# Optimization experiments

Measured on AMD Instinct MI355X. Metric: run time of the kernel, lower is better.

The kernel has to match this reference:

```python
import jax, jax.numpy as jnp
import numpy as np

E, A, K = 8192, 128, 512  # parallel_envs, num_agents, passengers per env
P = E * K                 # total passengers (global table rows)


def setup_inputs() -> dict:
    key = jax.random.key(0)
    k1, k2, k3, k4, k5, k6 = jax.random.split(key, 6)
    passengers = jax.random.normal(k1, (P, 11), dtype=jnp.float32)
    # column 0 is the env index of each passenger (used to gather timesteps)
    passengers = passengers.at[:, 0].set(jnp.repeat(jnp.arange(E, dtype=jnp.float32), K))
    accepts = jax.random.bernoulli(k2, 0.5, (E, A))
    picks = jax.random.bernoulli(k3, 0.3, (E, A))
    # env-partitioned global passenger indices: row e targets in [e*K, (e+1)*K)
    local_t = jax.random.randint(k4, (E, A), 0, K, dtype=jnp.int32)
    targets = jnp.arange(E, dtype=jnp.int32)[:, None] * K + local_t
    vectors = jax.random.normal(k5, (E, A, 4), dtype=jnp.float32)
    # give a quarter of agents zero src->dst distance so the pick branch fires
    vectors = vectors.at[:, : A // 4, 2:4].set(vectors[:, : A // 4, 0:2])
    # mark last 8 agent slots per env as invalid (all -100)
    vectors = vectors.at[:, -8:, :].set(-100.0)
    timesteps = jax.random.randint(k6, (E,), 0, 1000, dtype=jnp.int32)
    return {"passengers": passengers, "accepts": accepts, "picks": picks,
            "targets": targets, "vectors": vectors, "timesteps": timesteps}


def _distances(vectors):
    d = jnp.sqrt(((vectors[:, :, 0:2] - vectors[:, :, 2:4]) ** 2).sum(-1))
    return jnp.where((vectors == -100.0).all(-1), jnp.inf, d)


def _dup_mask(t, P):
    # torch: unique(return_inverse, return_counts) -> counts[inverse] > 1 & t != -100
    seg = jnp.where(t >= 0, t, P).ravel()  # -100 -> sentinel bucket P
    counts = jax.ops.segment_sum(jnp.ones(seg.shape, jnp.int32), seg, num_segments=P + 1)
    return (counts[seg].reshape(t.shape) > 1) & (t >= 0)


def reference(passengers, accepts, picks, targets, vectors, timesteps):
    E_, A_ = targets.shape
    P_ = passengers.shape[0]

    distances = _distances(vectors)
    accept_t = jnp.where(accepts, targets, -100)

    def cond(carry):
        t, _ = carry
        return _dup_mask(t, P_).any()

    def body(carry):
        t, d = carry
        dup = _dup_mask(t, P_)
        d = jnp.where(dup, d, jnp.inf)  # cumulative, as in torch
        keep = jnp.arange(A_)[None, :] == jnp.argmin(d, axis=1)[:, None]
        t = jnp.where(dup & ~keep, -100, t)
        return t, d

    accept_t, _ = jax.lax.while_loop(cond, body, (accept_t, distances))

    # scatter accept results into passenger table (at most one agent per passenger now)
    valid = accept_t >= 0
    seg = jnp.where(valid, accept_t, P_).ravel()
    accepted = jax.ops.segment_sum(valid.astype(jnp.int32).ravel(), seg, num_segments=P_ + 1)[:P_] > 0
    agent_ids = jnp.broadcast_to(jnp.arange(A_, dtype=jnp.int32)[None, :], (E_, A_))
    agent_of = jax.ops.segment_max(jnp.where(valid, agent_ids, -100).ravel(), seg, num_segments=P_ + 1)[:P_]
    ts = timesteps[passengers[:, 0].astype(jnp.int32)].astype(passengers.dtype)  # per-passenger timestep

    p = passengers
    p = p.at[:, 6].set(jnp.where(accepted, 1.0, p[:, 6]))
    p = p.at[:, 9].set(jnp.where(accepted, ts, p[:, 9]))
    p = p.at[:, 7].set(jnp.where(accepted, agent_of.astype(p.dtype), p[:, 7]))

    # pick transition: only zero-distance picks succeed
    d2 = _distances(vectors)
    pick_t = jnp.where(picks, targets, -100)
    pd = jnp.where(pick_t >= 0, d2, jnp.inf)
    pick_t = jnp.where(pd < 1e-6, pick_t, -100)
    pvalid = pick_t >= 0
    pseg = jnp.where(pvalid, pick_t, P_).ravel()
    picked = jax.ops.segment_sum(pvalid.astype(jnp.int32).ravel(), pseg, num_segments=P_ + 1)[:P_] > 0
    p = p.at[:, 6].set(jnp.where(picked, 2.0, p[:, 6]))
    p = p.at[:, 10].set(jnp.where(picked, ts, p[:, 10]))
    return p
```

## Files before the change

### kernel.cpp

```cpp
#include <hip/hip_runtime.h>

#define E_ENV 8192
#define A_AG  128
#define K_PASS 512
#define P_TOT (E_ENV * K_PASS)
#define N4    (P_TOT * 11 / 4)

__global__ __launch_bounds__(256) void k_copy(
    const float4* __restrict__ in, float4* __restrict__ out)
{
    int tid = blockIdx.x * 256 + threadIdx.x;
    out[tid] = in[tid];
}

__global__ __launch_bounds__(128) void k_env(
    const int* __restrict__ accepts, const int* __restrict__ picks,
    const int* __restrict__ targets, const float4* __restrict__ vectors,
    const int* __restrict__ timesteps, float* __restrict__ out)
{
    __shared__ int cnt[K_PASS];
    __shared__ float swv[2];
    __shared__ int   swi[2];

    const int e   = blockIdx.x;
    const int a   = threadIdx.x;
    const int gid = e * A_AG + a;

    #pragma unroll
    for (int j = 0; j < K_PASS / A_AG; ++j)
        cnt[a + j * A_AG] = 0;
    __syncthreads();

    float4 v = vectors[gid];
    bool invalid = (v.x == -100.0f) && (v.y == -100.0f) &&
                   (v.z == -100.0f) && (v.w == -100.0f);
    float dx = v.x - v.z, dy = v.y - v.w;
    float d = sqrtf(dx * dx + dy * dy);
    if (invalid) d = INFINITY;

    const int t     = targets[gid];
    const int tl    = t - e * K_PASS;
    const bool acc  = accepts[gid] != 0;
    const bool pick = picks[gid] != 0;

    int at = acc ? t : -100;
    if (at >= 0) atomicAdd(&cnt[tl], 1);
    __syncthreads();

    bool dup = (at >= 0) && (cnt[tl] > 1);
    float bv = dup ? d : INFINITY;
    int   bi = a;

    #pragma unroll
    for (int off = 32; off > 0; off >>= 1) {
        float ov = __shfl_xor(bv, off);
        int   oi = __shfl_xor(bi, off);
        if (ov < bv || (ov == bv && oi < bi)) { bv = ov; bi = oi; }
    }
    int wave = a >> 6;
    if ((a & 63) == 0) { swv[wave] = bv; swi[wave] = bi; }
    __syncthreads();
    float v0 = swv[0], v1 = swv[1];
    int   i0 = swi[0], i1 = swi[1];
    int bidx = (v1 < v0 || (v1 == v0 && i1 < i0)) ? i1 : i0;

    int f = (dup && a != bidx) ? -100 : at;

    const float tsf = (float)timesteps[e];

    if (f >= 0) {
        size_t b = (size_t)f * 11;
        out[b + 6] = 1.0f;
        out[b + 7] = (float)a;
        out[b + 9] = tsf;
    }
    __syncthreads();

    if (pick && d < 1e-6f) {
        size_t b = (size_t)t * 11;
        out[b + 6]  = 2.0f;
        out[b + 10] = tsf;
    }
}

extern "C" void kernel_launch(void* const* d_in, const int* in_sizes, int n_in,
                              void* d_out, int out_size, void* d_ws, size_t ws_size,
                              hipStream_t stream)
{
    const float* passengers = (const float*)d_in[0];
    const int*   accepts    = (const int*)d_in[1];
    const int*   picks      = (const int*)d_in[2];
    const int*   targets    = (const int*)d_in[3];
    const float* vectors    = (const float*)d_in[4];
    const int*   timesteps  = (const int*)d_in[5];
    float*       out        = (float*)d_out;

    k_copy<<<N4 / 256, 256, 0, stream>>>((const float4*)passengers, (float4*)out);

    k_env<<<E_ENV, A_AG, 0, stream>>>(accepts, picks, targets,
                                      (const float4*)vectors, timesteps, out);
}
```

Baseline: 344.8 us.

## Fuse passenger copy with per-env update into a single patched streaming kernel

Merges the bulk passenger-table copy and the per-environment accept/pick kernel into one kernel. Each block works out per-passenger accept agent and pick flags in shared memory, then streams its env's slice of the table as float4 and patches columns 6, 7, 9 and 10 in flight. This removes a second launch and the scattered read-modify-write traffic to global memory. In exchange there is per-element div/mod and branch work, and the copy now runs with only 128 threads per block.

```diff
diff --git a/kernel.cpp b/kernel.cpp
--- a/kernel.cpp
+++ b/kernel.cpp
@@ -1,24 +1,25 @@
 #include <hip/hip_runtime.h>
 
-#define E_ENV 8192
-#define A_AG  128
+#define E_ENV  8192
+#define A_AG   128
 #define K_PASS 512
-#define P_TOT (E_ENV * K_PASS)
-#define N4    (P_TOT * 11 / 4)
+#define ROW_F  11
+#define SLICE_F  (K_PASS * ROW_F)
+#define SLICE_V4 (SLICE_F / 4)
+#define ITERS    (SLICE_V4 / A_AG)
 
-__global__ __launch_bounds__(256) void k_copy(
-    const float4* __restrict__ in, float4* __restrict__ out)
+__global__ __launch_bounds__(128) void k_fused(
+    const float4* __restrict__ pass4,
+    const int*    __restrict__ accepts,
+    const int*    __restrict__ picks,
+    const int*    __restrict__ targets,
+    const float4* __restrict__ vectors,
+    const int*    __restrict__ timesteps,
+    float4*       __restrict__ out4)
 {
-    int tid = blockIdx.x * 256 + threadIdx.x;
-    out[tid] = in[tid];
-}
-
-__global__ __launch_bounds__(128) void k_env(
-    const int* __restrict__ accepts, const int* __restrict__ picks,
-    const int* __restrict__ targets, const float4* __restrict__ vectors,
-    const int* __restrict__ timesteps, float* __restrict__ out)
-{
-    __shared__ int cnt[K_PASS];
+    __shared__ int           cnt[K_PASS];
+    __shared__ int           agentOf[K_PASS];
+    __shared__ unsigned char pickF[K_PASS];
     __shared__ float swv[2];
     __shared__ int   swi[2];
 
@@ -27,8 +28,11 @@
     const int gid = e * A_AG + a;
 
     #pragma unroll
-    for (int j = 0; j < K_PASS / A_AG; ++j)
-        cnt[a + j * A_AG] = 0;
+    for (int j = 0; j < K_PASS / A_AG; ++j) {
+        cnt[a + j * A_AG]     = 0;
+        agentOf[a + j * A_AG] = -1;
+        pickF[a + j * A_AG]   = 0;
+    }
     __syncthreads();
 
     float4 v = vectors[gid];
@@ -38,8 +42,8 @@
     float d = sqrtf(dx * dx + dy * dy);
     if (invalid) d = INFINITY;
 
-    const int t     = targets[gid];
-    const int tl    = t - e * K_PASS;
+    const int  t    = targets[gid];
+    const int  tl   = t - e * K_PASS;
     const bool acc  = accepts[gid] != 0;
     const bool pick = picks[gid] != 0;
 
@@ -66,20 +70,42 @@
 
     int f = (dup && a != bidx) ? -100 : at;
 
+    if (f >= 0) agentOf[tl] = a;
+    if (pick && d < 1e-6f) pickF[tl] = 1;
+    __syncthreads();
+
     const float tsf = (float)timesteps[e];
 
-    if (f >= 0) {
-        size_t b = (size_t)f * 11;
-        out[b + 6] = 1.0f;
-        out[b + 7] = (float)a;
-        out[b + 9] = tsf;
-    }
-    __syncthreads();
+    const float4* src = pass4 + (size_t)e * SLICE_V4;
+    float4*       dst = out4  + (size_t)e * SLICE_V4;
 
-    if (pick && d < 1e-6f) {
-        size_t b = (size_t)t * 11;
-        out[b + 6]  = 2.0f;
-        out[b + 10] = tsf;
+    auto patch = [&](float val, unsigned row, int col) -> float {
+        if (col == 6) {
+            if (pickF[row]) return 2.0f;
+            if (agentOf[row] >= 0) return 1.0f;
+        } else if (col == 7) {
+            int ag = agentOf[row];
+            if (ag >= 0) return (float)ag;
+        } else if (col == 9) {
+            if (agentOf[row] >= 0) return tsf;
+        } else if (col == 10) {
+            if (pickF[row]) return tsf;
+        }
+        return val;
+    };
+
+    int idx = a;
+    #pragma unroll
+    for (int it = 0; it < ITERS; ++it, idx += A_AG) {
+        float4 x = src[idx];
+        unsigned g   = (unsigned)idx * 4u;
+        unsigned row = g / 11u;
+        int      col = (int)(g - row * 11u);
+        x.x = patch(x.x, row, col); if (++col == 11) { col = 0; ++row; }
+        x.y = patch(x.y, row, col); if (++col == 11) { col = 0; ++row; }
+        x.z = patch(x.z, row, col); if (++col == 11) { col = 0; ++row; }
+        x.w = patch(x.w, row, col);
+        dst[idx] = x;
     }
 }
 
@@ -95,8 +121,7 @@
     const int*   timesteps  = (const int*)d_in[5];
     float*       out        = (float*)d_out;
 
-    k_copy<<<N4 / 256, 256, 0, stream>>>((const float4*)passengers, (float4*)out);
-
-    k_env<<<E_ENV, A_AG, 0, stream>>>(accepts, picks, targets,
-                                      (const float4*)vectors, timesteps, out);
+    k_fused<<<E_ENV, A_AG, 0, stream>>>(
+        (const float4*)passengers, accepts, picks, targets,
+        (const float4*)vectors, timesteps, (float4*)out);
 }
```

Measured after the change: 346.8 us. No clear change (+0.6%).
